# Performance work log

Measured on AMD Instinct MI355X. Metric: run time of the kernel, lower is better.

## Reference

```python
import jax, jax.numpy as jnp
import numpy as np
import math

B, I, J = 4, 48, 384
D_TEXT, D_MEL, D_ATT = 512, 80, 128
NOISE_SCALE = 2.0
LOG_EPS = -1000.0


def setup_inputs() -> dict:
    key = jax.random.key(0)
    ks = jax.random.split(key, 8)
    return {
        "text_embeddings": jax.random.normal(ks[0], (B, I, D_TEXT), jnp.float32),
        "mel_embeddings": jax.random.normal(ks[1], (B, J, D_MEL), jnp.float32),
        "noise": jax.random.normal(ks[2], (B, I, J), jnp.float32),
        "W_text": jax.random.normal(ks[3], (D_TEXT, D_ATT), jnp.float32) * (1.0 / math.sqrt(D_TEXT)),
        "W_mel": jax.random.normal(ks[4], (D_MEL, D_ATT), jnp.float32) * (1.0 / math.sqrt(D_MEL)),
        "b_mel": jnp.zeros((D_ATT,), jnp.float32),
        "v_w": jax.random.normal(ks[5], (D_ATT,), jnp.float32) * math.sqrt(1.0 / D_ATT),
        "v_b": jnp.zeros((), jnp.float32),
        "text_mask": jnp.ones((B, I), bool),
        "mel_mask": jnp.ones((B, J), bool),
    }


def reference(text_embeddings, mel_embeddings, noise, W_text, W_mel, b_mel, v_w, v_b, text_mask, mel_mask):
    # ---- compute_energy: additive (Bahdanau) attention, v(tanh(Wt x_i + Wm m_j + b)) ----
    pt = text_embeddings @ W_text                    # (B,I,D_att), no bias
    pm = mel_embeddings @ W_mel + b_mel              # (B,J,D_att)
    energy = jnp.tanh(pt[:, :, None, :] + pm[:, None, :, :]) @ v_w + v_b   # (B,I,J)
    energy = energy + NOISE_SCALE * noise            # apply_noise

    tlen = text_mask.sum(1)                          # (B,)
    mlen = mel_mask.sum(1)                           # (B,)
    ii = jnp.arange(I)
    jj = jnp.arange(J)

    # ---- invalid mask for P(B_i = j | B_{i-1} = k): monotonic (j >= k), padding, force last ----
    inv = (jj[:, None] < jj[None, :])[None, None, :, :]                       # j < k invalid
    inv = inv | (~text_mask)[:, :, None, None]
    inv = inv | (~mel_mask)[:, None, :, None] | (~mel_mask)[:, None, None, :]
    last = (ii[None, :] == tlen[:, None] - 1)[:, :, None] & (jj[None, :] != mlen[:, None] - 1)[:, None, :]
    inv = inv | last[:, :, :, None]                                           # force_assign_last=True

    e4 = jnp.where(inv, LOG_EPS, energy[..., None])                           # (B,I,J,K)
    lcp = e4 - jax.nn.logsumexp(e4, axis=2, keepdims=True)                    # log P(j | i, k)
    geq = jax.lax.cumlogsumexp(lcp, axis=2, reverse=True)                     # log P(B_i >= j | k)
    geq = jnp.where(inv, LOG_EPS, geq)

    # ---- compute_forward_pass: banded DP over text positions (log domain) ----
    width = J - I + 2
    lcp_pad = jnp.concatenate([lcp, jnp.full((B, I, 1, J), LOG_EPS, lcp.dtype)], axis=2)  # (B,I,J+1,K)
    row0 = jnp.full((B, J + 1), -jnp.inf, lcp.dtype).at[:, 0].set(0.0)

    def step(prev, i):
        # B_ij[:, i, i : J-I+i+2] = LSE_k( B_ij[:, i-1, k] + lcp[:, i-1, i-1 : J-I+i+1, k] )
        blk = jax.lax.dynamic_slice(lcp_pad, (0, i - 1, i - 1, 0), (B, 1, width, J))[:, 0]  # (B,width,K)
        vals = jax.nn.logsumexp(prev[:, None, :-1] + blk, axis=2)                            # (B,width)
        row = jnp.full((B, J + 2), -jnp.inf, lcp.dtype)
        row = jax.lax.dynamic_update_slice(row, vals, (0, i))[:, :J + 1]
        return row, row

    _, rows = jax.lax.scan(step, row0, jnp.arange(1, I + 1))                  # (I,B,J+1)
    # Bij_forward = B_ij[:, :-1, :-1]
    Bij = jnp.concatenate([row0[:, None, :], jnp.moveaxis(rows, 0, 1)[:, :I - 1]], axis=1)[:, :, :-1]  # (B,I,J)

    # ---- compute_interval_probability: soft[b,i,j] = LSE_k( Bij[b,i,k] + geq[b,i,j,k] ) ----
    soft = jax.nn.logsumexp(Bij[:, :, None, :] + geq, axis=3)                 # (B,I,J)

    expanded = jnp.einsum('bij,bid->bjd', jnp.exp(soft), text_embeddings)     # (B,J,D_text)
    return soft, expanded
```

## Files before the change

kernel.cpp:

```cpp
#include <hip/hip_runtime.h>
#include <hip/hip_bf16.h>
#include <math.h>

#define B_ 4
#define I_ 48
#define J_ 384
#define DT_ 512
#define DM_ 80
#define DA_ 128
#define WIDTH_ 338
#define NEG (-1e30f)
#define LOG2E 1.4426950408889634f
#define LN2 0.6931471805599453f
#define LOGEPS2 (-1442.6950408889634f)
#define VPT 6

typedef float f32x4 __attribute__((ext_vector_type(4)));
typedef float f32x2 __attribute__((ext_vector_type(2)));

__device__ __forceinline__ float fexp2(float x) { return __builtin_amdgcn_exp2f(x); }
__device__ __forceinline__ float flog2(float x) { return __builtin_amdgcn_logf(x); }

template<int CTRL, int RMASK>
__device__ __forceinline__ float dppf(float x) {
    return __int_as_float(__builtin_amdgcn_update_dpp(
        __float_as_int(NEG), __float_as_int(x), CTRL, RMASK, 0xF, false));
}
__device__ __forceinline__ float rlane(float x, int l) {
    return __int_as_float(__builtin_amdgcn_readlane(__float_as_int(x), l));
}

__device__ __forceinline__ float lse2(float a, float b) {
    float m = fmaxf(a, b);
    float d = a - b;
    return m + flog2(1.0f + fexp2(-fabsf(d)));
}

__device__ __forceinline__ float wave_scan_fwd(float x) {
    x = lse2(x, dppf<0x111, 0xF>(x));
    x = lse2(x, dppf<0x112, 0xF>(x));
    x = lse2(x, dppf<0x114, 0xF>(x));
    x = lse2(x, dppf<0x118, 0xF>(x));
    x = lse2(x, dppf<0x142, 0xA>(x));
    x = lse2(x, dppf<0x143, 0xC>(x));
    return x;
}
__device__ __forceinline__ float wave_scan_rev(float x, int lane) {
    x = lse2(x, dppf<0x101, 0xF>(x));
    x = lse2(x, dppf<0x102, 0xF>(x));
    x = lse2(x, dppf<0x104, 0xF>(x));
    x = lse2(x, dppf<0x108, 0xF>(x));
    float s16 = rlane(x, 16), s32 = rlane(x, 32), s48 = rlane(x, 48);
    float a  = lse2(s32, s48);
    float b2 = lse2(s16, a);
    int row = lane >> 4;
    float pre = (row == 0) ? b2 : (row == 1) ? a : (row == 2) ? s48 : NEG;
    return lse2(x, pre);
}

__device__ __forceinline__ float tanh_fast(float x) {
    float t = fexp2(x * (2.0f * LOG2E));
    return fmaf(-2.0f, __builtin_amdgcn_rcpf(t + 1.0f), 1.0f);
}

__global__ __launch_bounds__(128) void proj_kernel(
        const float* __restrict__ text, const float* __restrict__ mel,
        const float* __restrict__ Wt, const float* __restrict__ Wm,
        const float* __restrict__ bm, float* __restrict__ pt, float* __restrict__ pm) {
    int blk = blockIdx.x;
    int d = threadIdx.x;
    __shared__ float sx[DT_];
    if (blk < B_ * I_) {
        const float* x = text + blk * DT_;
        for (int e = d; e < DT_; e += DA_) sx[e] = x[e];
        __syncthreads();
        float acc = 0.f;
        #pragma unroll 8
        for (int e = 0; e < DT_; ++e) acc += sx[e] * Wt[e * DA_ + d];
        pt[blk * DA_ + d] = acc;
    } else {
        int r = blk - B_ * I_;
        const float* x = mel + r * DM_;
        if (d < DM_) sx[d] = x[d];
        __syncthreads();
        float acc = bm[d];
        #pragma unroll 8
        for (int e = 0; e < DM_; ++e) acc += sx[e] * Wm[e * DA_ + d];
        pm[r * DA_ + d] = acc;
    }
}

__global__ __launch_bounds__(384) void energy_kernel(
        const float* __restrict__ pt, const float* __restrict__ pm,
        const float* __restrict__ vw, const float* __restrict__ vb,
        const float* __restrict__ noise, float* __restrict__ EZ) {
    int bi = blockIdx.x;
    int b = bi / I_, i = bi % I_;
    int t = threadIdx.x;
    int w = t >> 6, lane = t & 63;
    __shared__ float sPt[DA_];
    __shared__ float sPR[8];
    __shared__ float sLast;
    if (t < DA_) sPt[t] = pt[bi * DA_ + t];
    __syncthreads();
    const float4* pmr4 = (const float4*)(pm + (size_t)(b * J_ + t) * DA_);
    float acc = 0.f;
    #pragma unroll 8
    for (int q = 0; q < DA_ / 4; ++q) {
        float4 v = pmr4[q];
        acc += vw[4 * q + 0] * tanh_fast(sPt[4 * q + 0] + v.x);
        acc += vw[4 * q + 1] * tanh_fast(sPt[4 * q + 1] + v.y);
        acc += vw[4 * q + 2] * tanh_fast(sPt[4 * q + 2] + v.z);
        acc += vw[4 * q + 3] * tanh_fast(sPt[4 * q + 3] + v.w);
    }
    float e = (acc + vb[0] + 2.0f * noise[bi * J_ + t]) * LOG2E;

    float y = wave_scan_rev(e, lane);
    if (lane == 0) sPR[w] = y;
    if (t == J_ - 1) sLast = e;
    __syncthreads();
    float preR = NEG;
    #pragma unroll
    for (int ww = 1; ww < 6; ++ww) if (ww > w) preR = lse2(preR, sPR[ww]);
    float z = lse2(y, preR);
    if (i == I_ - 1) z = sLast;
    float2 o; o.x = e; o.y = z;
    ((float2*)(EZ + (size_t)bi * J_ * 2))[t] = o;
}

#define WAITV_(n) asm volatile("s_waitcnt vmcnt(" #n ")" ::: "memory")
#define WAITV(n) do { WAITV_(n); __builtin_amdgcn_sched_barrier(0); } while (0)

#define LOAD3(S, rowexpr) do { \
    const float* _a = EZb + (size_t)(rowexpr) * (2 * J_) + t * 12; \
    asm volatile("global_load_dwordx4 %0, %3, off\n\t" \
                 "global_load_dwordx4 %1, %3, off offset:16\n\t" \
                 "global_load_dwordx4 %2, %3, off offset:32" \
                 : "=&v"(S##0), "=&v"(S##1), "=&v"(S##2) \
                 : "v"(_a) : "memory"); } while (0)

#define STORE42(addr, q, dd) \
    asm volatile("global_store_dwordx4 %2, %0, off\n\t" \
                 "global_store_dwordx2 %2, %1, off offset:16" \
                 :: "v"(q), "v"(dd), "v"(addr) : "memory")

#define BODY(iexpr, NW, S, DOLOAD, lrow) do { \
    const int i_ = (iexpr); \
    WAITV(NW); \
    float e0 = S##0[0], z0 = S##0[1], e1 = S##0[2], z1 = S##0[3]; \
    float e2 = S##1[0], z2 = S##1[1], e3 = S##1[2], z3 = S##1[3]; \
    float e4 = S##2[0], z4 = S##2[1], e5 = S##2[2], z5 = S##2[3]; \
    if (DOLOAD) LOAD3(S, lrow); \
    float D0 = prev[0] - z0, D1 = prev[1] - z1, D2 = prev[2] - z2; \
    float D3 = prev[3] - z3, D4 = prev[4] - z4, D5 = prev[5] - z5; \
    float s01 = lse2(D0, D1), p23 = lse2(D2, D3), p45 = lse2(D4, D5); \
    float f2 = lse2(s01, D2), f3 = lse2(s01, p23); \
    float f4 = lse2(f3, D4),  f5 = lse2(f3, p45); \
    float Sf  = wave_scan_fwd(f5); \
    float exF = dppf<0x138, 0xF>(Sf);       \
    float flo = rlane(Sf, 63) + LOGEPS2;    \
    float eP  = dppf<0x138, 0xF>(e5);       \
    float v0 = lse2(eP + exF,            flo); \
    float v1 = lse2(e0 + lse2(D0,  exF), flo); \
    float v2 = lse2(e1 + lse2(s01, exF), flo); \
    float v3 = lse2(e2 + lse2(f2,  exF), flo); \
    float v4 = lse2(e3 + lse2(f3,  exF), flo); \
    float v5 = lse2(e4 + lse2(f4,  exF), flo); \
    int lo = i_, hi = i_ + WIDTH_; \
    prev[0] = (p0 + 0 >= lo && p0 + 0 < hi) ? v0 : NEG; \
    prev[1] = (p0 + 1 >= lo && p0 + 1 < hi) ? v1 : NEG; \
    prev[2] = (p0 + 2 >= lo && p0 + 2 < hi) ? v2 : NEG; \
    prev[3] = (p0 + 3 >= lo && p0 + 3 < hi) ? v3 : NEG; \
    prev[4] = (p0 + 4 >= lo && p0 + 4 < hi) ? v4 : NEG; \
    prev[5] = (p0 + 5 >= lo && p0 + 5 < hi) ? v5 : NEG; \
    { f32x4 q = {prev[0], prev[1], prev[2], prev[3]}; \
      f32x2 dd = {prev[4], prev[5]}; \
      float* _ba = Bb + i_ * J_ + p0; \
      STORE42(_ba, q, dd); } \
} while (0)

__global__ __launch_bounds__(384) void dpsoft_kernel(
        const float* __restrict__ EZ, float* __restrict__ Bij,
        float* __restrict__ soft) {
    int blk = blockIdx.x;
    int t = threadIdx.x;
    int w = t >> 6, lane = t & 63;
    const float* EZb = EZ + (size_t)blk * I_ * J_ * 2;
    float* Bb = Bij + (size_t)blk * I_ * J_;
    float* softB = soft + (size_t)blk * I_ * J_;

    if (t < 64) {
        int p0 = t * VPT;
        float prev[VPT];
        #pragma unroll
        for (int r = 0; r < VPT; ++r) prev[r] = (p0 + r == 0) ? 0.f : NEG;

        { f32x4 q = {prev[0], prev[1], prev[2], prev[3]};
          f32x2 dd = {prev[4], prev[5]};
          float* _ba = Bb + p0;
          STORE42(_ba, q, dd); }

        f32x4 A0, A1, A2, B0, B1, B2, C0, C1, C2;
        LOAD3(A, 0); LOAD3(B, 1); LOAD3(C, 2);

        BODY(1, 6,  A, 1, 3);
        BODY(2, 8,  B, 1, 4);
        BODY(3, 10, C, 1, 5);
        #pragma unroll 1
        for (int i = 4; i <= 43; i += 3) {
            BODY(i,     12, A, 1, i + 2);
            BODY(i + 1, 12, B, 1, i + 3);
            BODY(i + 2, 12, C, 1, i + 4);
        }
        BODY(46, 12, A, 0, 0);
        BODY(47, 9,  B, 0, 0);
    }
    __syncthreads();

    int p0 = lane * VPT;
    #pragma unroll 1
    for (int rr = 0; rr < 8; ++rr) {
        int row = w * 8 + rr;
        const float* Brow = Bb + (size_t)row * J_;
        float Bv0 = Brow[p0 + 0], Bv1 = Brow[p0 + 1], Bv2 = Brow[p0 + 2];
        float Bv3 = Brow[p0 + 3], Bv4 = Brow[p0 + 4], Bv5 = Brow[p0 + 5];
        float q23 = lse2(Bv2, Bv3), q45 = lse2(Bv4, Bv5);
        float g5 = Bv5, g4 = q45;
        float g3 = lse2(Bv3, q45), g2 = lse2(q23, q45);
        float g1 = lse2(Bv1, g2),  g0 = lse2(Bv0, g1);
        float Sg = wave_scan_rev(g0, lane);
        float* orow = softB + (size_t)row * J_ + p0;
        if (row == I_ - 1) {
            float tot = rlane(Sg, 0);
            #pragma unroll
            for (int r = 0; r < VPT; ++r)
                orow[r] = ((p0 + r == J_ - 1) ? tot : tot + LOGEPS2) * LN2;
        } else {
            float exG = dppf<0x130, 0xF>(Sg);
            const float* Erow = EZb + (size_t)row * 2 * J_;
            float Zv0 = Erow[(p0 + 0) * 2 + 1], Zv1 = Erow[(p0 + 1) * 2 + 1];
            float Zv2 = Erow[(p0 + 2) * 2 + 1], Zv3 = Erow[(p0 + 3) * 2 + 1];
            float Zv4 = Erow[(p0 + 4) * 2 + 1], Zv5 = Erow[(p0 + 5) * 2 + 1];
            float C0 = Bv0 - Zv0, C1 = Bv1 - Zv1, C2 = Bv2 - Zv2;
            float C3 = Bv3 - Zv3, C4 = Bv4 - Zv4, C5 = Bv5 - Zv5;
            float s01 = lse2(C0, C1), p23 = lse2(C2, C3), p45 = lse2(C4, C5);
            float f0 = C0, f1 = s01, f2 = lse2(s01, C2), f3 = lse2(s01, p23);
            float f4 = lse2(f3, C4), f5 = lse2(f3, p45);
            float Sf = wave_scan_fwd(f5);
            float exF = dppf<0x138, 0xF>(Sf);
            float o0 = lse2(Zv0 + lse2(f0, exF), lse2(g1, exG) + LOGEPS2);
            float o1 = lse2(Zv1 + lse2(f1, exF), lse2(g2, exG) + LOGEPS2);
            float o2 = lse2(Zv2 + lse2(f2, exF), lse2(g3, exG) + LOGEPS2);
            float o3 = lse2(Zv3 + lse2(f3, exF), lse2(g4, exG) + LOGEPS2);
            float o4 = lse2(Zv4 + lse2(f4, exF), lse2(g5, exG) + LOGEPS2);
            float o5 = lse2(Zv5 + lse2(f5, exF), exG + LOGEPS2);
            orow[0] = o0 * LN2; orow[1] = o1 * LN2; orow[2] = o2 * LN2;
            orow[3] = o3 * LN2; orow[4] = o4 * LN2; orow[5] = o5 * LN2;
        }
    }
}

__global__ __launch_bounds__(512) void expand_kernel(
        const float* __restrict__ soft, const float* __restrict__ text,
        float* __restrict__ out) {
    int bj = blockIdx.x;
    int b = bj / J_, j = bj % J_;
    int d = threadIdx.x;
    __shared__ float p[I_];
    if (d < I_) p[d] = __expf(soft[(b * I_ + d) * J_ + j]);
    __syncthreads();
    float acc = 0.f;
    #pragma unroll
    for (int i = 0; i < I_; ++i) acc += p[i] * text[(b * I_ + i) * DT_ + d];
    out[bj * DT_ + d] = acc;
}

extern "C" void kernel_launch(void* const* d_in, const int* in_sizes, int n_in,
                              void* d_out, int out_size, void* d_ws, size_t ws_size,
                              hipStream_t stream) {
    const float* text  = (const float*)d_in[0];
    const float* mel   = (const float*)d_in[1];
    const float* noise = (const float*)d_in[2];
    const float* Wt    = (const float*)d_in[3];
    const float* Wm    = (const float*)d_in[4];
    const float* bm    = (const float*)d_in[5];
    const float* vw    = (const float*)d_in[6];
    const float* vb    = (const float*)d_in[7];

    float* ws  = (float*)d_ws;
    float* EZ  = ws;
    float* pt  = EZ + B_ * I_ * J_ * 2;
    float* pm  = pt + B_ * I_ * DA_;
    float* Bij = pm + B_ * J_ * DA_;

    float* soft     = (float*)d_out;
    float* expanded = soft + B_ * I_ * J_;

    proj_kernel<<<B_ * (I_ + J_), 128, 0, stream>>>(text, mel, Wt, Wm, bm, pt, pm);
    energy_kernel<<<B_ * I_, 384, 0, stream>>>(pt, pm, vw, vb, noise, EZ);
    dpsoft_kernel<<<B_, 384, 0, stream>>>(EZ, Bij, soft);
    expand_kernel<<<B_ * J_, 512, 0, stream>>>(soft, text, expanded);
}
```

Before: 71.80 us.

## Carry log-sum-exp as (max, scale) pairs in DP scan to drop per-step logs

The serial forward DP recurrence now carries each log-sum-exp value as a (max, linear scale) pair, so every combine needs one exp2 and an FMA instead of an exp2 plus a log2. log2 is applied only when a row is written to Bij. The second phase runs 512 threads (8 waves of 6 rows instead of 6 waves of 8), and its Bij and EZ reads are vectorized. The pair form doubles the DPP shuffles in the wave scan and the register pressure on the single-wave critical path, and it adds select logic in every combine.

```diff
diff --git a/kernel.cpp b/kernel.cpp
--- a/kernel.cpp
+++ b/kernel.cpp
@@ -26,6 +26,11 @@
     return __int_as_float(__builtin_amdgcn_update_dpp(
         __float_as_int(NEG), __float_as_int(x), CTRL, RMASK, 0xF, false));
 }
+template<int CTRL, int RMASK>
+__device__ __forceinline__ float dpps(float x) {
+    return __int_as_float(__builtin_amdgcn_update_dpp(
+        0x3f800000, __float_as_int(x), CTRL, RMASK, 0xF, false));
+}
 __device__ __forceinline__ float rlane(float x, int l) {
     return __int_as_float(__builtin_amdgcn_readlane(__float_as_int(x), l));
 }
@@ -34,6 +39,27 @@
     float m = fmaxf(a, b);
     float d = a - b;
     return m + flog2(1.0f + fexp2(-fabsf(d)));
+}
+
+struct fpair { float m, s; };
+__device__ __forceinline__ fpair mkp(float m, float s) { fpair p; p.m = m; p.s = s; return p; }
+__device__ __forceinline__ fpair pcomb(fpair A, fpair B) {
+    float M = fmaxf(A.m, B.m);
+    float d = A.m - B.m;
+    float sc = fexp2(-fabsf(d));
+    float hi = (d >= 0.f) ? A.s : B.s;
+    float lo = (d >= 0.f) ? B.s : A.s;
+    return mkp(M, fmaf(lo, sc, hi));
+}
+__device__ __forceinline__ fpair wscan_fwd_p(fpair x) {
+    fpair t;
+    t.m = dppf<0x111, 0xF>(x.m); t.s = dpps<0x111, 0xF>(x.s); x = pcomb(x, t);
+    t.m = dppf<0x112, 0xF>(x.m); t.s = dpps<0x112, 0xF>(x.s); x = pcomb(x, t);
+    t.m = dppf<0x114, 0xF>(x.m); t.s = dpps<0x114, 0xF>(x.s); x = pcomb(x, t);
+    t.m = dppf<0x118, 0xF>(x.m); t.s = dpps<0x118, 0xF>(x.s); x = pcomb(x, t);
+    t.m = dppf<0x142, 0xA>(x.m); t.s = dpps<0x142, 0xA>(x.s); x = pcomb(x, t);
+    t.m = dppf<0x143, 0xC>(x.m); t.s = dpps<0x143, 0xC>(x.s); x = pcomb(x, t);
+    return x;
 }
 
 __device__ __forceinline__ float wave_scan_fwd(float x) {
@@ -144,42 +170,49 @@
                  "global_store_dwordx2 %2, %1, off offset:16" \
                  :: "v"(q), "v"(dd), "v"(addr) : "memory")
 
-#define BODY(iexpr, NW, S, DOLOAD, lrow) do { \
+#define PBODY(iexpr, NW, S, DOLOAD, lrow) do { \
     const int i_ = (iexpr); \
     WAITV(NW); \
     float e0 = S##0[0], z0 = S##0[1], e1 = S##0[2], z1 = S##0[3]; \
     float e2 = S##1[0], z2 = S##1[1], e3 = S##1[2], z3 = S##1[3]; \
     float e4 = S##2[0], z4 = S##2[1], e5 = S##2[2], z5 = S##2[3]; \
     if (DOLOAD) LOAD3(S, lrow); \
-    float D0 = prev[0] - z0, D1 = prev[1] - z1, D2 = prev[2] - z2; \
-    float D3 = prev[3] - z3, D4 = prev[4] - z4, D5 = prev[5] - z5; \
-    float s01 = lse2(D0, D1), p23 = lse2(D2, D3), p45 = lse2(D4, D5); \
-    float f2 = lse2(s01, D2), f3 = lse2(s01, p23); \
-    float f4 = lse2(f3, D4),  f5 = lse2(f3, p45); \
-    float Sf  = wave_scan_fwd(f5); \
-    float exF = dppf<0x138, 0xF>(Sf);       \
-    float flo = rlane(Sf, 63) + LOGEPS2;    \
-    float eP  = dppf<0x138, 0xF>(e5);       \
-    float v0 = lse2(eP + exF,            flo); \
-    float v1 = lse2(e0 + lse2(D0,  exF), flo); \
-    float v2 = lse2(e1 + lse2(s01, exF), flo); \
-    float v3 = lse2(e2 + lse2(f2,  exF), flo); \
-    float v4 = lse2(e3 + lse2(f3,  exF), flo); \
-    float v5 = lse2(e4 + lse2(f4,  exF), flo); \
-    int lo = i_, hi = i_ + WIDTH_; \
-    prev[0] = (p0 + 0 >= lo && p0 + 0 < hi) ? v0 : NEG; \
-    prev[1] = (p0 + 1 >= lo && p0 + 1 < hi) ? v1 : NEG; \
-    prev[2] = (p0 + 2 >= lo && p0 + 2 < hi) ? v2 : NEG; \
-    prev[3] = (p0 + 3 >= lo && p0 + 3 < hi) ? v3 : NEG; \
-    prev[4] = (p0 + 4 >= lo && p0 + 4 < hi) ? v4 : NEG; \
-    prev[5] = (p0 + 5 >= lo && p0 + 5 < hi) ? v5 : NEG; \
-    { f32x4 q = {prev[0], prev[1], prev[2], prev[3]}; \
-      f32x2 dd = {prev[4], prev[5]}; \
+    fpair D0 = mkp(prev[0].m - z0, prev[0].s); \
+    fpair D1 = mkp(prev[1].m - z1, prev[1].s); \
+    fpair D2 = mkp(prev[2].m - z2, prev[2].s); \
+    fpair D3 = mkp(prev[3].m - z3, prev[3].s); \
+    fpair D4 = mkp(prev[4].m - z4, prev[4].s); \
+    fpair D5 = mkp(prev[5].m - z5, prev[5].s); \
+    fpair s01 = pcomb(D0, D1), p23 = pcomb(D2, D3), p45 = pcomb(D4, D5); \
+    fpair f2 = pcomb(s01, D2), f3 = pcomb(s01, p23); \
+    fpair f4 = pcomb(f3, D4),  f5 = pcomb(f3, p45); \
+    fpair Sf = wscan_fwd_p(f5); \
+    fpair exF; exF.m = dppf<0x138, 0xF>(Sf.m); exF.s = dpps<0x138, 0xF>(Sf.s); \
+    fpair flo = mkp(rlane(Sf.m, 63) + LOGEPS2, rlane(Sf.s, 63));   \
+    float eP = dppf<0x138, 0xF>(e5); \
+    fpair c1 = pcomb(D0, exF),  c2 = pcomb(s01, exF); \
+    fpair c3 = pcomb(f2, exF),  c4 = pcomb(f3, exF),  c5 = pcomb(f4, exF); \
+    fpair v0 = pcomb(mkp(eP + exF.m, exF.s), flo); \
+    fpair v1 = pcomb(mkp(e0 + c1.m, c1.s), flo); \
+    fpair v2 = pcomb(mkp(e1 + c2.m, c2.s), flo); \
+    fpair v3 = pcomb(mkp(e2 + c3.m, c3.s), flo); \
+    fpair v4 = pcomb(mkp(e3 + c4.m, c4.s), flo); \
+    fpair v5 = pcomb(mkp(e4 + c5.m, c5.s), flo); \
+    int lo_ = i_, hi_ = i_ + WIDTH_; \
+    prev[0] = (p0 + 0 >= lo_ && p0 + 0 < hi_) ? v0 : mkp(NEG, 1.f); \
+    prev[1] = (p0 + 1 >= lo_ && p0 + 1 < hi_) ? v1 : mkp(NEG, 1.f); \
+    prev[2] = (p0 + 2 >= lo_ && p0 + 2 < hi_) ? v2 : mkp(NEG, 1.f); \
+    prev[3] = (p0 + 3 >= lo_ && p0 + 3 < hi_) ? v3 : mkp(NEG, 1.f); \
+    prev[4] = (p0 + 4 >= lo_ && p0 + 4 < hi_) ? v4 : mkp(NEG, 1.f); \
+    prev[5] = (p0 + 5 >= lo_ && p0 + 5 < hi_) ? v5 : mkp(NEG, 1.f); \
+    { f32x4 q = {prev[0].m + flog2(prev[0].s), prev[1].m + flog2(prev[1].s), \
+                 prev[2].m + flog2(prev[2].s), prev[3].m + flog2(prev[3].s)}; \
+      f32x2 dd = {prev[4].m + flog2(prev[4].s), prev[5].m + flog2(prev[5].s)}; \
       float* _ba = Bb + i_ * J_ + p0; \
       STORE42(_ba, q, dd); } \
 } while (0)
 
-__global__ __launch_bounds__(384) void dpsoft_kernel(
+__global__ __launch_bounds__(512) void dpsoft_kernel(
         const float* __restrict__ EZ, float* __restrict__ Bij,
         float* __restrict__ soft) {
     int blk = blockIdx.x;
@@ -191,39 +224,40 @@
 
     if (t < 64) {
         int p0 = t * VPT;
-        float prev[VPT];
+        fpair prev[VPT];
         #pragma unroll
-        for (int r = 0; r < VPT; ++r) prev[r] = (p0 + r == 0) ? 0.f : NEG;
-
-        { f32x4 q = {prev[0], prev[1], prev[2], prev[3]};
-          f32x2 dd = {prev[4], prev[5]};
+        for (int r = 0; r < VPT; ++r) prev[r] = mkp((p0 + r == 0) ? 0.f : NEG, 1.f);
+
+        { f32x4 q = {prev[0].m, prev[1].m, prev[2].m, prev[3].m};
+          f32x2 dd = {prev[4].m, prev[5].m};
           float* _ba = Bb + p0;
           STORE42(_ba, q, dd); }
 
         f32x4 A0, A1, A2, B0, B1, B2, C0, C1, C2;
         LOAD3(A, 0); LOAD3(B, 1); LOAD3(C, 2);
 
-        BODY(1, 6,  A, 1, 3);
-        BODY(2, 8,  B, 1, 4);
-        BODY(3, 10, C, 1, 5);
+        PBODY(1, 6,  A, 1, 3);
+        PBODY(2, 8,  B, 1, 4);
+        PBODY(3, 10, C, 1, 5);
         #pragma unroll 1
         for (int i = 4; i <= 43; i += 3) {
-            BODY(i,     12, A, 1, i + 2);
-            BODY(i + 1, 12, B, 1, i + 3);
-            BODY(i + 2, 12, C, 1, i + 4);
+            PBODY(i,     12, A, 1, i + 2);
+            PBODY(i + 1, 12, B, 1, i + 3);
+            PBODY(i + 2, 12, C, 1, i + 4);
         }
-        BODY(46, 12, A, 0, 0);
-        BODY(47, 9,  B, 0, 0);
+        PBODY(46, 12, A, 0, 0);
+        PBODY(47, 9,  B, 0, 0);
     }
     __syncthreads();
 
     int p0 = lane * VPT;
-    #pragma unroll 1
-    for (int rr = 0; rr < 8; ++rr) {
-        int row = w * 8 + rr;
-        const float* Brow = Bb + (size_t)row * J_;
-        float Bv0 = Brow[p0 + 0], Bv1 = Brow[p0 + 1], Bv2 = Brow[p0 + 2];
-        float Bv3 = Brow[p0 + 3], Bv4 = Brow[p0 + 4], Bv5 = Brow[p0 + 5];
+    #pragma unroll 2
+    for (int rr = 0; rr < 6; ++rr) {
+        int row = w * 6 + rr;
+        const f32x2* B2 = (const f32x2*)(Bb + (size_t)row * J_ + p0);
+        f32x2 ba = B2[0], bb2 = B2[1], bc = B2[2];
+        float Bv0 = ba[0], Bv1 = ba[1], Bv2 = bb2[0];
+        float Bv3 = bb2[1], Bv4 = bc[0], Bv5 = bc[1];
         float q23 = lse2(Bv2, Bv3), q45 = lse2(Bv4, Bv5);
         float g5 = Bv5, g4 = q45;
         float g3 = lse2(Bv3, q45), g2 = lse2(q23, q45);
@@ -237,10 +271,10 @@
                 orow[r] = ((p0 + r == J_ - 1) ? tot : tot + LOGEPS2) * LN2;
         } else {
             float exG = dppf<0x130, 0xF>(Sg);
-            const float* Erow = EZb + (size_t)row * 2 * J_;
-            float Zv0 = Erow[(p0 + 0) * 2 + 1], Zv1 = Erow[(p0 + 1) * 2 + 1];
-            float Zv2 = Erow[(p0 + 2) * 2 + 1], Zv3 = Erow[(p0 + 3) * 2 + 1];
-            float Zv4 = Erow[(p0 + 4) * 2 + 1], Zv5 = Erow[(p0 + 5) * 2 + 1];
+            const f32x4* E4 = (const f32x4*)(EZb + (size_t)row * 2 * J_ + p0 * 2);
+            f32x4 ea = E4[0], eb = E4[1], ec = E4[2];
+            float Zv0 = ea[1], Zv1 = ea[3], Zv2 = eb[1];
+            float Zv3 = eb[3], Zv4 = ec[1], Zv5 = ec[3];
             float C0 = Bv0 - Zv0, C1 = Bv1 - Zv1, C2 = Bv2 - Zv2;
             float C3 = Bv3 - Zv3, C4 = Bv4 - Zv4, C5 = Bv5 - Zv5;
             float s01 = lse2(C0, C1), p23 = lse2(C2, C3), p45 = lse2(C4, C5);
@@ -298,6 +332,6 @@
 
     proj_kernel<<<B_ * (I_ + J_), 128, 0, stream>>>(text, mel, Wt, Wm, bm, pt, pm);
     energy_kernel<<<B_ * I_, 384, 0, stream>>>(pt, pm, vw, vb, noise, EZ);
-    dpsoft_kernel<<<B_, 384, 0, stream>>>(EZ, Bij, soft);
+    dpsoft_kernel<<<B_, 512, 0, stream>>>(EZ, Bij, soft);
     expand_kernel<<<B_ * J_, 512, 0, stream>>>(soft, text, expanded);
 }
```

New measurement: 72.86 us. About the same (+1.5%).
